# Performance work log

Hardware: AMD Instinct MI355X
Metric: run time of the kernel (lower is better)

Reference implementation:

```python
import jax, jax.numpy as jnp
import numpy as np

VOCAB, E, HID, K = 32000, 256, 512, 9
B, T = 32, 512
H = HID // 2  # per-direction hidden


def _lstm_dir(x, w_ih, w_hh, b_ih, b_hh):
    # x: [B,T,E]; w_ih: [4H,E]; w_hh: [4H,H]. PyTorch gate order i,f,g,o.
    xp = jnp.einsum('bte,ge->btg', x, w_ih) + b_ih + b_hh  # [B,T,4H]
    h0 = jnp.zeros((x.shape[0], w_hh.shape[1]), x.dtype)
    c0 = jnp.zeros_like(h0)

    def step(carry, xt):
        h, c = carry
        g = xt + h @ w_hh.T
        i, f, gg, o = jnp.split(g, 4, axis=-1)
        c = jax.nn.sigmoid(f) * c + jax.nn.sigmoid(i) * jnp.tanh(gg)
        h = jax.nn.sigmoid(o) * jnp.tanh(c)
        return (h, c), h

    _, hs = jax.lax.scan(step, (h0, c0), jnp.swapaxes(xp, 0, 1))
    return jnp.swapaxes(hs, 0, 1)  # [B,T,H]


def _crf_nll_mean(emissions, tags, mask, trans, start_trans, end_trans):
    # emissions: [B,T,K]; tags: [B,T] int; mask: [B,T] bool (mask[:,0] must be 1)
    mf = mask.astype(emissions.dtype)
    # numerator: score of gold path
    em_tag = jnp.take_along_axis(emissions, tags[..., None], axis=2)[..., 0]  # [B,T]
    tr = trans[tags[:, :-1], tags[:, 1:]]  # [B,T-1]
    score = start_trans[tags[:, 0]] + em_tag[:, 0]
    score = score + ((tr + em_tag[:, 1:]) * mf[:, 1:]).sum(axis=1)
    last_idx = mf.sum(axis=1).astype(jnp.int32) - 1
    last_tags = jnp.take_along_axis(tags, last_idx[:, None], axis=1)[:, 0]
    score = score + end_trans[last_tags]
    # partition: forward algorithm (log-sum-exp semiring scan)
    alpha0 = start_trans + emissions[:, 0]  # [B,K]

    def step(alpha, inp):
        em_t, m_t = inp  # [B,K], [B]
        nxt = jax.nn.logsumexp(alpha[:, :, None] + trans[None] + em_t[:, None, :], axis=1)
        return jnp.where(m_t[:, None], nxt, alpha), None

    alpha, _ = jax.lax.scan(
        step, alpha0,
        (jnp.swapaxes(emissions[:, 1:], 0, 1), jnp.swapaxes(mask[:, 1:], 0, 1)))
    logZ = jax.nn.logsumexp(alpha + end_trans, axis=1)  # [B]
    llh = score - logZ
    return -jnp.mean(llh)


def setup_inputs() -> dict:
    key = jax.random.key(0)
    ks = jax.random.split(key, 16)
    s = 0.05
    return {
        'input_ids': jax.random.randint(ks[0], (B, T), 0, VOCAB, dtype=jnp.int32),
        'tags': jax.random.randint(ks[1], (B, T), 0, K, dtype=jnp.int32),
        'mask': jnp.ones((B, T), dtype=bool),
        'emb_table': jax.random.normal(ks[2], (VOCAB, E), jnp.float32) * s,
        'w_ih_f': jax.random.normal(ks[3], (4 * H, E), jnp.float32) * s,
        'w_hh_f': jax.random.normal(ks[4], (4 * H, H), jnp.float32) * s,
        'b_ih_f': jax.random.normal(ks[5], (4 * H,), jnp.float32) * s,
        'b_hh_f': jax.random.normal(ks[6], (4 * H,), jnp.float32) * s,
        'w_ih_b': jax.random.normal(ks[7], (4 * H, E), jnp.float32) * s,
        'w_hh_b': jax.random.normal(ks[8], (4 * H, H), jnp.float32) * s,
        'b_ih_b': jax.random.normal(ks[9], (4 * H,), jnp.float32) * s,
        'b_hh_b': jax.random.normal(ks[10], (4 * H,), jnp.float32) * s,
        'w_out': jax.random.normal(ks[11], (K, HID), jnp.float32) * s,
        'b_out': jax.random.normal(ks[12], (K,), jnp.float32) * s,
        'trans': jax.random.normal(ks[13], (K, K), jnp.float32) * s,
        'start_trans': jax.random.normal(ks[14], (K,), jnp.float32) * s,
        'end_trans': jax.random.normal(ks[15], (K,), jnp.float32) * s,
    }


def reference(input_ids, tags, mask, emb_table,
              w_ih_f, w_hh_f, b_ih_f, b_hh_f,
              w_ih_b, w_hh_b, b_ih_b, b_hh_b,
              w_out, b_out, trans, start_trans, end_trans):
    embeds = emb_table[input_ids]  # [B,T,E]
    h_f = _lstm_dir(embeds, w_ih_f, w_hh_f, b_ih_f, b_hh_f)
    h_b = _lstm_dir(embeds[:, ::-1], w_ih_b, w_hh_b, b_ih_b, b_hh_b)[:, ::-1]
    lstm_out = jnp.concatenate([h_f, h_b], axis=-1)  # [B,T,HID]
    emissions = jnp.einsum('bth,kh->btk', lstm_out, w_out) + b_out
    return _crf_nll_mean(emissions, tags, mask, trans, start_trans, end_trans)
```

## Files before the change

kernel.cpp:

```cpp
#include <hip/hip_runtime.h>
#include <hip/hip_bf16.h>

#define B_ 32
#define T_ 512
#define E_ 256
#define Hh 256
#define G4 1024
#define K_ 9

__device__ float g_WihT[2][E_][G4];
__device__ float g_WhhT[2][Hh][G4];
__device__ float g_xp[2][B_][T_][G4];
__device__ float g_hout[2][B_][T_][Hh];
__device__ float g_em[B_ * T_ * K_];
__device__ float g_score[B_];
__device__ unsigned long long g_hx[2][64][4][64];

__global__ __launch_bounds__(256) void transpose_w(
    const float* __restrict__ wihf, const float* __restrict__ wihb,
    const float* __restrict__ whhf, const float* __restrict__ whhb) {
  int wg = blockIdx.x;
  int mat = wg >> 8;
  int c = wg & 255;
  const float* src = (mat == 0) ? wihf : (mat == 1) ? wihb : (mat == 2) ? whhf : whhb;
  float* dst = (mat == 0) ? &g_WihT[0][c][0] : (mat == 1) ? &g_WihT[1][c][0]
             : (mat == 2) ? &g_WhhT[0][c][0] : &g_WhhT[1][c][0];
#pragma unroll
  for (int k = 0; k < 4; ++k) {
    int g = threadIdx.x + 256 * k;
    dst[g] = src[g * 256 + c];
  }
}

__global__ __launch_bounds__(256) void reset_tags() {
  unsigned long long* p = &g_hx[0][0][0][0];
  p[blockIdx.x * 256 + threadIdx.x] = 0ull;
}

__global__ __launch_bounds__(256) void xp_gemm(
    const int* __restrict__ ids, const float* __restrict__ emb,
    const float* __restrict__ bihf, const float* __restrict__ bhhf,
    const float* __restrict__ bihb, const float* __restrict__ bhhb) {
  __shared__ float AsT[64][72];
  __shared__ float Bs[64][64];
  int tid = threadIdx.x;
  int n0 = blockIdx.x * 64;
  int m0 = blockIdx.y * 64;
  int dir = m0 >> 14;
  int rem = m0 & 16383;
  int b = rem >> 9;
  int t0 = rem & 511;
  int ty = tid >> 4, tx = tid & 15;
  int lr = tid >> 2;
  int lk = (tid & 3) << 4;
  int tt = t0 + lr;
  int colt = dir ? (T_ - 1 - tt) : tt;
  const float* arow = emb + (size_t)ids[b * T_ + colt] * E_;
  const float* WT = &g_WihT[dir][0][0];
  float acc[4][4] = {};
  for (int k0 = 0; k0 < E_; k0 += 64) {
#pragma unroll
    for (int q = 0; q < 4; ++q) {
      float4 v = *(const float4*)(arow + k0 + lk + 4 * q);
      AsT[lk + 4 * q + 0][lr] = v.x;
      AsT[lk + 4 * q + 1][lr] = v.y;
      AsT[lk + 4 * q + 2][lr] = v.z;
      AsT[lk + 4 * q + 3][lr] = v.w;
      float4 w = *(const float4*)(WT + (size_t)(k0 + lr) * G4 + n0 + lk + 4 * q);
      *(float4*)&Bs[lr][lk + 4 * q] = w;
    }
    __syncthreads();
#pragma unroll 8
    for (int kk = 0; kk < 64; ++kk) {
      float4 av = *(const float4*)&AsT[kk][ty * 4];
      float4 bv = *(const float4*)&Bs[kk][tx * 4];
      float a[4] = {av.x, av.y, av.z, av.w};
      float bb[4] = {bv.x, bv.y, bv.z, bv.w};
#pragma unroll
      for (int i = 0; i < 4; ++i)
#pragma unroll
        for (int j = 0; j < 4; ++j) acc[i][j] += a[i] * bb[j];
    }
    __syncthreads();
  }
  const float* bih = dir ? bihb : bihf;
  const float* bhh = dir ? bhhb : bhhf;
  float* xpb = &g_xp[dir][b][0][0];
  int g0 = n0 + tx * 4;
#pragma unroll
  for (int i = 0; i < 4; ++i) {
    int t = t0 + ty * 4 + i;
    float4 v;
    v.x = acc[i][0] + bih[g0 + 0] + bhh[g0 + 0];
    v.y = acc[i][1] + bih[g0 + 1] + bhh[g0 + 1];
    v.z = acc[i][2] + bih[g0 + 2] + bhh[g0 + 2];
    v.w = acc[i][3] + bih[g0 + 3] + bhh[g0 + 3];
    *(float4*)&xpb[(size_t)t * G4 + g0] = v;
  }
}

__global__ __launch_bounds__(512, 2) void lstm_kernel() {
  int blk = blockIdx.x;
  int chain = blk & 63;
  int member = blk >> 6;
  int dir = chain & 1, b = chain >> 1;
  int tid = threadIdx.x;
  int col = tid >> 1;
  int half = tid & 1;
  int gg = col >> 6;
  int jj = col & 63;
  int gate_g = gg * 256 + member * 64 + jj;
  __shared__ float h_lds[256];
  __shared__ float gate_lds[256];

  float w[128];
  const float* Wcol = &g_WhhT[dir][half * 128][0] + gate_g;
#pragma unroll
  for (int k = 0; k < 128; ++k) w[k] = Wcol[(size_t)k * G4];
#pragma unroll
  for (int k = 0; k < 128; ++k) asm volatile("" : "+v"(w[k]));

  if (tid < 256) h_lds[tid] = 0.f;
  const float* xp = &g_xp[dir][b][0][0];
  float* hout = &g_hout[dir][b][0][0];
  float cst = 0.f;
  float xp_cur = xp[gate_g];
  __syncthreads();

  for (int t = 0; t < T_; ++t) {
    float xp_next = (t < T_ - 1) ? xp[(size_t)(t + 1) * G4 + gate_g] : 0.f;
    float a0 = xp_cur, a1 = 0.f, a2 = 0.f, a3 = 0.f;
    const float* hp = &h_lds[half * 128];
#pragma unroll
    for (int k = 0; k < 128; k += 8) {
      float4 hA = *(const float4*)&hp[k];
      float4 hB = *(const float4*)&hp[k + 4];
      a0 += w[k + 0] * hA.x + w[k + 1] * hA.y;
      a1 += w[k + 2] * hA.z + w[k + 3] * hA.w;
      a2 += w[k + 4] * hB.x + w[k + 5] * hB.y;
      a3 += w[k + 6] * hB.z + w[k + 7] * hB.w;
    }
    float acc = (a0 + a1) + (a2 + a3);
    acc += __shfl_xor(acc, 1);
    if (half == 0) gate_lds[col] = acc;
    __syncthreads();

    int par = t & 1;
    if (tid < 64) {
      float iv = gate_lds[tid];
      float fv = gate_lds[64 + tid];
      float gv = gate_lds[128 + tid];
      float ov = gate_lds[192 + tid];
      float si = 1.f / (1.f + expf(-iv));
      float sf = 1.f / (1.f + expf(-fv));
      float so = 1.f / (1.f + expf(-ov));
      cst = sf * cst + si * tanhf(gv);
      float h = so * tanhf(cst);
      h_lds[member * 64 + tid] = h;
      int tr = dir ? (T_ - 1 - t) : t;
      hout[(size_t)tr * Hh + member * 64 + tid] = h;
      if (t < T_ - 1) {
        unsigned long long pk =
            ((unsigned long long)(unsigned)(t + 1) << 32) |
            (unsigned long long)__float_as_uint(h);
        __hip_atomic_store(&g_hx[par][chain][member][tid], pk,
                           __ATOMIC_RELAXED, __HIP_MEMORY_SCOPE_AGENT);
      }
    } else if (tid < 256 && t < T_ - 1) {
      int idx = tid - 64;
      int rm = idx >> 6;
      rm += (rm >= member);
      int j = idx & 63;
      unsigned long long v;
      int cnt = 0;
      do {
        v = __hip_atomic_load(&g_hx[par][chain][rm][j],
                              __ATOMIC_RELAXED, __HIP_MEMORY_SCOPE_AGENT);
      } while ((unsigned)(v >> 32) != (unsigned)(t + 1) && ++cnt < (1 << 18));
      h_lds[rm * 64 + j] = __uint_as_float((unsigned)v);
    }
    __syncthreads();
    xp_cur = xp_next;
  }
}

__global__ __launch_bounds__(256) void emis_kernel(const float* __restrict__ wout,
                                                   const float* __restrict__ bout) {
  __shared__ float wout_s[K_ * 512];
  __shared__ float hs[8][512];
  int tid = threadIdx.x;
  int bt0 = blockIdx.x * 8;
  for (int i = tid; i < K_ * 512; i += 256) wout_s[i] = wout[i];
  for (int i = tid; i < 8 * 512; i += 256) {
    int r = i >> 9, c = i & 511;
    int bt = bt0 + r;
    int b = bt >> 9, t = bt & 511;
    hs[r][c] = (c < 256) ? g_hout[0][b][t][c] : g_hout[1][b][t][c - 256];
  }
  __syncthreads();
  if (tid < 8 * K_) {
    int r = tid / K_, k = tid % K_;
    float acc = bout[k];
    const float* w = &wout_s[k * 512];
    const float* h = &hs[r][0];
#pragma unroll 8
    for (int c = 0; c < 512; ++c) acc += h[c] * w[c];
    g_em[(size_t)(bt0 + r) * K_ + k] = acc;
  }
}

__global__ __launch_bounds__(256) void crf_score(const int* __restrict__ tags,
                                                 const float* __restrict__ trans,
                                                 const float* __restrict__ strans,
                                                 const float* __restrict__ etrans) {
  int b = blockIdx.x;
  int tid = threadIdx.x;
  float s = 0.f;
  for (int t = tid; t < T_; t += 256) {
    int tg = tags[b * T_ + t];
    s += g_em[(size_t)(b * T_ + t) * K_ + tg];
    if (t == 0)
      s += strans[tg];
    else
      s += trans[tags[b * T_ + t - 1] * K_ + tg];
    if (t == T_ - 1) s += etrans[tg];
  }
  __shared__ float red[256];
  red[tid] = s;
  __syncthreads();
  for (int off = 128; off > 0; off >>= 1) {
    if (tid < off) red[tid] += red[tid + off];
    __syncthreads();
  }
  if (tid == 0) g_score[b] = red[0];
}

__global__ __launch_bounds__(320) void crf_alpha(const float* __restrict__ trans,
                                                 const float* __restrict__ strans,
                                                 const float* __restrict__ etrans,
                                                 float* __restrict__ out) {
  __shared__ float al[B_][12];
  __shared__ float tr_s[K_ * K_];
  __shared__ float lz_s[B_];
  int tid = threadIdx.x;
  if (tid < K_ * K_) tr_s[tid] = trans[tid];
  bool act = tid < B_ * K_;
  int b = tid / K_, j = tid % K_;
  if (act) al[b][j] = strans[j] + g_em[(size_t)(b * T_) * K_ + j];
  __syncthreads();
  for (int t = 1; t < T_; ++t) {
    float nxt = 0.f;
    if (act) {
      float m = -1e30f;
#pragma unroll
      for (int i = 0; i < K_; ++i) m = fmaxf(m, al[b][i] + tr_s[i * K_ + j]);
      float s = 0.f;
#pragma unroll
      for (int i = 0; i < K_; ++i) s += expf(al[b][i] + tr_s[i * K_ + j] - m);
      nxt = m + logf(s) + g_em[(size_t)(b * T_ + t) * K_ + j];
    }
    __syncthreads();
    if (act) al[b][j] = nxt;
    __syncthreads();
  }
  if (tid < B_) {
    float m = -1e30f;
#pragma unroll
    for (int i = 0; i < K_; ++i) m = fmaxf(m, al[tid][i] + etrans[i]);
    float s = 0.f;
#pragma unroll
    for (int i = 0; i < K_; ++i) s += expf(al[tid][i] + etrans[i] - m);
    lz_s[tid] = m + logf(s);
  }
  __syncthreads();
  if (tid == 0) {
    float acc = 0.f;
    for (int bb = 0; bb < B_; ++bb) acc += lz_s[bb] - g_score[bb];
    out[0] = acc / (float)B_;
  }
}

extern "C" void kernel_launch(void* const* d_in, const int* in_sizes, int n_in,
                              void* d_out, int out_size, void* d_ws, size_t ws_size,
                              hipStream_t stream) {
  const int* ids = (const int*)d_in[0];
  const int* tags = (const int*)d_in[1];
  const float* emb = (const float*)d_in[3];
  const float* wihf = (const float*)d_in[4];
  const float* whhf = (const float*)d_in[5];
  const float* bihf = (const float*)d_in[6];
  const float* bhhf = (const float*)d_in[7];
  const float* wihb = (const float*)d_in[8];
  const float* whhb = (const float*)d_in[9];
  const float* bihb = (const float*)d_in[10];
  const float* bhhb = (const float*)d_in[11];
  const float* wout = (const float*)d_in[12];
  const float* bout = (const float*)d_in[13];
  const float* trans = (const float*)d_in[14];
  const float* strans = (const float*)d_in[15];
  const float* etrans = (const float*)d_in[16];
  float* out = (float*)d_out;

  hipLaunchKernelGGL(transpose_w, dim3(1024), dim3(256), 0, stream, wihf, wihb, whhf, whhb);
  hipLaunchKernelGGL(reset_tags, dim3(128), dim3(256), 0, stream);
  hipLaunchKernelGGL(xp_gemm, dim3(16, 512), dim3(256), 0, stream, ids, emb, bihf, bhhf, bihb, bhhb);
  hipLaunchKernelGGL(lstm_kernel, dim3(256), dim3(512), 0, stream);
  hipLaunchKernelGGL(emis_kernel, dim3(2048), dim3(256), 0, stream, wout, bout);
  hipLaunchKernelGGL(crf_score, dim3(32), dim3(256), 0, stream, tags, trans, strans, etrans);
  hipLaunchKernelGGL(crf_alpha, dim3(1), dim3(320), 0, stream, trans, strans, etrans, out);
}
```

Before: 1.939 ms.

## Repartition LSTM recurrence across hidden slices with batched sequences per workgroup

```diff
diff --git a/kernel.cpp b/kernel.cpp
--- a/kernel.cpp
+++ b/kernel.cpp
@@ -8,13 +8,18 @@
 #define G4 1024
 #define K_ 9
 
+#define NH 8
+#define NB 8
+#define NG 32
+#define WPAD 260
+
 __device__ float g_WihT[2][E_][G4];
 __device__ float g_WhhT[2][Hh][G4];
 __device__ float g_xp[2][B_][T_][G4];
 __device__ float g_hout[2][B_][T_][Hh];
 __device__ float g_em[B_ * T_ * K_];
 __device__ float g_score[B_];
-__device__ unsigned long long g_hx[2][64][4][64];
+__device__ unsigned long long g_hx[2][2][4][32][64];
 
 __global__ __launch_bounds__(256) void transpose_w(
     const float* __restrict__ wihf, const float* __restrict__ wihb,
@@ -33,7 +38,7 @@
 }
 
 __global__ __launch_bounds__(256) void reset_tags() {
-  unsigned long long* p = &g_hx[0][0][0][0];
+  unsigned long long* p = &g_hx[0][0][0][0][0];
   p[blockIdx.x * 256 + threadIdx.x] = 0ull;
 }
 
@@ -99,88 +104,116 @@
   }
 }
 
-__global__ __launch_bounds__(512, 2) void lstm_kernel() {
-  int blk = blockIdx.x;
-  int chain = blk & 63;
-  int member = blk >> 6;
-  int dir = chain & 1, b = chain >> 1;
-  int tid = threadIdx.x;
-  int col = tid >> 1;
-  int half = tid & 1;
-  int gg = col >> 6;
-  int jj = col & 63;
-  int gate_g = gg * 256 + member * 64 + jj;
-  __shared__ float h_lds[256];
-  __shared__ float gate_lds[256];
-
-  float w[128];
-  const float* Wcol = &g_WhhT[dir][half * 128][0] + gate_g;
-#pragma unroll
-  for (int k = 0; k < 128; ++k) w[k] = Wcol[(size_t)k * G4];
-#pragma unroll
-  for (int k = 0; k < 128; ++k) asm volatile("" : "+v"(w[k]));
-
-  if (tid < 256) h_lds[tid] = 0.f;
-  const float* xp = &g_xp[dir][b][0][0];
-  float* hout = &g_hout[dir][b][0][0];
+#define FMH(i, q, A)                                                     \
+  {                                                                      \
+    float4 hv_ = *(const float4*)&h_lds[q][cb16 + 4 * (i)];              \
+    A += wv##i.x * hv_.x + wv##i.y * hv_.y + wv##i.z * hv_.z +           \
+         wv##i.w * hv_.w;                                                \
+  }
+#define FMI(i)                                                           \
+  {                                                                      \
+    float4 wv##i = *(const float4*)&w_lds[fg][cb16 + 4 * (i)];           \
+    FMH(i, 0, a0) FMH(i, 1, a1) FMH(i, 2, a2) FMH(i, 3, a3)              \
+    FMH(i, 4, a4) FMH(i, 5, a5) FMH(i, 6, a6) FMH(i, 7, a7)              \
+  }
+
+__global__ __launch_bounds__(512) void lstm_kernel(const float* __restrict__ whhf,
+                                                   const float* __restrict__ whhb) {
+  int wgid = blockIdx.x;
+  int dir = wgid >> 7;
+  int bg = (wgid >> 5) & 3;
+  int hblk = wgid & 31;
+  int tid = threadIdx.x;
+
+  __shared__ float w_lds[NG][WPAD];
+  __shared__ float h_lds[NB][256];
+  __shared__ float part[16][NB][NG];
+  __shared__ float gate_lds[NG][9];
+
+  const float* whh = dir ? whhb : whhf;
+  {
+    int g = tid >> 4, seg = tid & 15;
+    int gg = g >> 3, jj = g & 7;
+    int gglob = gg * 256 + hblk * NH + jj;
+    const float* src = whh + (size_t)gglob * 256 + seg * 16;
+#pragma unroll
+    for (int k = 0; k < 4; ++k)
+      *(float4*)&w_lds[g][seg * 16 + 4 * k] = *(const float4*)(src + 4 * k);
+  }
+  for (int i = tid; i < NB * 256; i += 512) (&h_lds[0][0])[i] = 0.f;
+
+  int fg = tid & 31;
+  int fcb = tid >> 5;
+  int cb16 = fcb * 16;
+  int rg = tid & 31, rq = tid >> 5;
+  int gglob_r = (rg >> 3) * 256 + hblk * NH + (rg & 7);
+  const float* xpb = (tid < 256) ? &g_xp[dir][bg * NB + rq][0][0] : nullptr;
+  float xq = (tid < 256) ? xpb[gglob_r] : 0.f;
   float cst = 0.f;
-  float xp_cur = xp[gate_g];
   __syncthreads();
 
   for (int t = 0; t < T_; ++t) {
-    float xp_next = (t < T_ - 1) ? xp[(size_t)(t + 1) * G4 + gate_g] : 0.f;
-    float a0 = xp_cur, a1 = 0.f, a2 = 0.f, a3 = 0.f;
-    const float* hp = &h_lds[half * 128];
-#pragma unroll
-    for (int k = 0; k < 128; k += 8) {
-      float4 hA = *(const float4*)&hp[k];
-      float4 hB = *(const float4*)&hp[k + 4];
-      a0 += w[k + 0] * hA.x + w[k + 1] * hA.y;
-      a1 += w[k + 2] * hA.z + w[k + 3] * hA.w;
-      a2 += w[k + 4] * hB.x + w[k + 5] * hB.y;
-      a3 += w[k + 6] * hB.z + w[k + 7] * hB.w;
-    }
-    float acc = (a0 + a1) + (a2 + a3);
-    acc += __shfl_xor(acc, 1);
-    if (half == 0) gate_lds[col] = acc;
+    float a0 = 0.f, a1 = 0.f, a2 = 0.f, a3 = 0.f,
+          a4 = 0.f, a5 = 0.f, a6 = 0.f, a7 = 0.f;
+    FMI(0) FMI(1) FMI(2) FMI(3)
+    part[fcb][0][fg] = a0; part[fcb][1][fg] = a1;
+    part[fcb][2][fg] = a2; part[fcb][3][fg] = a3;
+    part[fcb][4][fg] = a4; part[fcb][5][fg] = a5;
+    part[fcb][6][fg] = a6; part[fcb][7][fg] = a7;
+    __syncthreads();
+
+    if (tid < 256) {
+      float s = xq;
+#pragma unroll
+      for (int cb = 0; cb < 16; ++cb) s += part[cb][rq][rg];
+      gate_lds[rg][rq] = s;
+      if (t < T_ - 1) xq = xpb[(size_t)(t + 1) * G4 + gglob_r];
+    }
     __syncthreads();
 
     int par = t & 1;
     if (tid < 64) {
-      float iv = gate_lds[tid];
-      float fv = gate_lds[64 + tid];
-      float gv = gate_lds[128 + tid];
-      float ov = gate_lds[192 + tid];
+      int jj = tid & 7, aq = tid >> 3;
+      float iv = gate_lds[jj][aq];
+      float fv = gate_lds[8 + jj][aq];
+      float gv = gate_lds[16 + jj][aq];
+      float ov = gate_lds[24 + jj][aq];
       float si = 1.f / (1.f + expf(-iv));
       float sf = 1.f / (1.f + expf(-fv));
       float so = 1.f / (1.f + expf(-ov));
       cst = sf * cst + si * tanhf(gv);
       float h = so * tanhf(cst);
-      h_lds[member * 64 + tid] = h;
+      int hg = hblk * NH + jj;
+      h_lds[aq][hg] = h;
       int tr = dir ? (T_ - 1 - t) : t;
-      hout[(size_t)tr * Hh + member * 64 + tid] = h;
+      g_hout[dir][bg * NB + aq][tr][hg] = h;
       if (t < T_ - 1) {
         unsigned long long pk =
             ((unsigned long long)(unsigned)(t + 1) << 32) |
             (unsigned long long)__float_as_uint(h);
-        __hip_atomic_store(&g_hx[par][chain][member][tid], pk,
+        __hip_atomic_store(&g_hx[par][dir][bg][hblk][tid], pk,
                            __ATOMIC_RELAXED, __HIP_MEMORY_SCOPE_AGENT);
       }
-    } else if (tid < 256 && t < T_ - 1) {
-      int idx = tid - 64;
-      int rm = idx >> 6;
-      rm += (rm >= member);
-      int j = idx & 63;
-      unsigned long long v;
-      int cnt = 0;
-      do {
-        v = __hip_atomic_load(&g_hx[par][chain][rm][j],
-                              __ATOMIC_RELAXED, __HIP_MEMORY_SCOPE_AGENT);
-      } while ((unsigned)(v >> 32) != (unsigned)(t + 1) && ++cnt < (1 << 18));
-      h_lds[rm * 64 + j] = __uint_as_float((unsigned)v);
-    }
-    __syncthreads();
-    xp_cur = xp_next;
+    }
+    if (t < T_ - 1) {
+#pragma unroll
+      for (int r = 0; r < 4; ++r) {
+        int idx = r * 512 + tid;
+        if (idx < 31 * 64) {
+          int rhb = idx >> 6;
+          rhb += (rhb >= hblk);
+          int sub = idx & 63;
+          unsigned long long v;
+          int cnt = 0;
+          do {
+            v = __hip_atomic_load(&g_hx[par][dir][bg][rhb][sub],
+                                  __ATOMIC_RELAXED, __HIP_MEMORY_SCOPE_AGENT);
+          } while ((unsigned)(v >> 32) != (unsigned)(t + 1) && ++cnt < (1 << 18));
+          h_lds[sub >> 3][rhb * NH + (sub & 7)] = __uint_as_float((unsigned)v);
+        }
+      }
+    }
+    __syncthreads();
   }
 }
 
@@ -304,7 +337,7 @@
   hipLaunchKernelGGL(transpose_w, dim3(1024), dim3(256), 0, stream, wihf, wihb, whhf, whhb);
   hipLaunchKernelGGL(reset_tags, dim3(128), dim3(256), 0, stream);
   hipLaunchKernelGGL(xp_gemm, dim3(16, 512), dim3(256), 0, stream, ids, emb, bihf, bhhf, bihb, bhhb);
-  hipLaunchKernelGGL(lstm_kernel, dim3(256), dim3(512), 0, stream);
+  hipLaunchKernelGGL(lstm_kernel, dim3(256), dim3(512), 0, stream, whhf, whhb);
   hipLaunchKernelGGL(emis_kernel, dim3(2048), dim3(256), 0, stream, wout, bout);
   hipLaunchKernelGGL(crf_score, dim3(32), dim3(256), 0, stream, tags, trans, strans, etrans);
   hipLaunchKernelGGL(crf_alpha, dim3(1), dim3(320), 0, stream, trans, strans, etrans, out);
```

Result: slower. 2.405 ms (+24.0%).
